# Kernel tuning notes

Hardware: AMD Instinct MI355X
Metric: run time of the kernel (lower is better)

The kernel has to match this reference:

```python
import jax, jax.numpy as jnp
import numpy as np

V, M, E, H = 20000, 32, 128, 4      # vocab, max news per word, embed dim, heads
N, L, C = 8192, 64, 128             # num news, max sent len, cnn out channels
KS = (3, 4, 5)


def setup_inputs() -> dict:
    key = jax.random.key(0)
    ks = jax.random.split(key, 12)
    s = 0.02
    return {
        "word2news": jax.random.randint(ks[0], (V, M), 0, N),
        "word2news_len": jax.random.randint(ks[1], (V,), 0, M),
        "news_words": jax.random.randint(ks[2], (N, L), 0, V),
        "news_embed_table": jax.random.normal(ks[3], (N, E), jnp.float32) * s,
        "in_proj_w": jax.random.normal(ks[4], (3 * E, E), jnp.float32) * s,
        "in_proj_b": jnp.zeros((3 * E,), jnp.float32),
        "out_proj_w": jax.random.normal(ks[5], (E, E), jnp.float32) * s,
        "out_proj_b": jnp.zeros((E,), jnp.float32),
        "conv_w3": jax.random.normal(ks[6], (C, E, 3), jnp.float32) * s,
        "conv_b3": jnp.zeros((C,), jnp.float32),
        "conv_w4": jax.random.normal(ks[7], (C, E, 4), jnp.float32) * s,
        "conv_b4": jnp.zeros((C,), jnp.float32),
        "conv_w5": jax.random.normal(ks[8], (C, E, 5), jnp.float32) * s,
        "conv_b5": jnp.zeros((C,), jnp.float32),
        "fc_w": jax.random.normal(ks[9], (E, len(KS) * C), jnp.float32) * s,
        "fc_b": jnp.zeros((E,), jnp.float32),
    }


def _conv1d(x, w, b):
    # x: [N, E, L]  w: [C, E, k]  -> [N, C, L-k+1]
    y = jax.lax.conv_general_dilated(x, w, (1,), "VALID",
                                     dimension_numbers=("NCH", "OIH", "NCH"))
    return y + b[None, :, None]


def _word_embeds(word2news, word2news_len, table, in_w, in_b, out_w, out_b):
    # Batched version of the per-word loop: masked mean query + 1-query MHA.
    mask = jnp.arange(M)[None, :] < word2news_len[:, None]          # [V, M]
    ctx = table[word2news]                                           # [V, M, E]
    cnt = jnp.maximum(word2news_len, 1).astype(ctx.dtype)[:, None]
    q = jnp.sum(jnp.where(mask[:, :, None], ctx, 0.0), axis=1) / cnt  # [V, E]
    wq, wk, wv = jnp.split(in_w, 3, axis=0)
    bq, bk, bv = jnp.split(in_b, 3, axis=0)
    Dh = E // H
    qh = (q @ wq.T + bq).reshape(V, H, Dh)
    kh = (ctx @ wk.T + bk).reshape(V, M, H, Dh)
    vh = (ctx @ wv.T + bv).reshape(V, M, H, Dh)
    scores = jnp.einsum("vhd,vmhd->vhm", qh, kh) / jnp.sqrt(jnp.asarray(Dh, ctx.dtype))
    scores = jnp.where(mask[:, None, :], scores, -1e9)
    attn = jax.nn.softmax(scores, axis=-1)
    o = jnp.einsum("vhm,vmhd->vhd", attn, vh).reshape(V, E)
    o = o @ out_w.T + out_b
    # words with no news stay zero, matching the zeros-init table in torch
    return jnp.where((word2news_len > 0)[:, None], o, 0.0)            # [V, E]


def reference(word2news, word2news_len, news_words, news_embed_table,
              in_proj_w, in_proj_b, out_proj_w, out_proj_b,
              conv_w3, conv_b3, conv_w4, conv_b4, conv_w5, conv_b5,
              fc_w, fc_b):
    word_embeds = _word_embeds(word2news, word2news_len, news_embed_table,
                               in_proj_w, in_proj_b, out_proj_w, out_proj_b)
    doc = word_embeds[news_words]                 # [N, L, E]
    x = doc.transpose(0, 2, 1)                    # [N, E, L]
    pooled = [jnp.max(jax.nn.relu(_conv1d(x, w, b)), axis=2)
              for w, b in ((conv_w3, conv_b3), (conv_w4, conv_b4), (conv_w5, conv_b5))]
    feats = jnp.concatenate(pooled, axis=1)       # [N, 3*C]; dropout=identity (eval)
    return feats @ fc_w.T + fc_b                  # [N, E]
```

## Files before the change

kernel.cpp:

```cpp
#include <hip/hip_runtime.h>
#include <math.h>

#define V_WORDS 20000
#define MM 32
#define EE 128
#define HH 4
#define DHH 32
#define NN 8192
#define LL 64
#define CC 128

typedef short bf16x8 __attribute__((ext_vector_type(8)));
typedef float f32x4 __attribute__((ext_vector_type(4)));
typedef unsigned short u16;
typedef unsigned int u32;

__device__ __forceinline__ u16 f2bf(float x) {
    u32 u = __float_as_uint(x);
    u32 r = (u + 0x7FFFu + ((u >> 16) & 1u)) >> 16;
    return (u16)r;
}
__device__ __forceinline__ float bflo(u32 u) { return __uint_as_float(u << 16); }
__device__ __forceinline__ float bfhi(u32 u) { return __uint_as_float(u & 0xFFFF0000u); }

__global__ __launch_bounds__(256)
void pack_weights(const float* __restrict__ w3,
                  const float* __restrict__ w4,
                  const float* __restrict__ w5,
                  u16* __restrict__ Bpack)
{
    const int s = blockIdx.x;
    const int t = threadIdx.x;
    const int lane = t & 63;

    const float* src;
    int K, sl;
    if (s < 12)      { src = w3; K = 3; sl = s; }
    else if (s < 28) { src = w4; K = 4; sl = s - 12; }
    else             { src = w5; K = 5; sl = s - 28; }
    const int j  = sl >> 2;
    const int e0 = (sl & 3) * 32;

    for (int nt = (t >> 6); nt < 8; nt += 4) {
        const int c = nt * 16 + (lane & 15);
        const int kb = (lane >> 4) * 8;
        u16 vals[8];
        #pragma unroll
        for (int i = 0; i < 8; ++i) {
            const int e = e0 + kb + i;
            vals[i] = f2bf(src[(c * EE + e) * K + j]);
        }
        u16* dst = Bpack + (((size_t)s * 8 + nt) * 64 + lane) * 8;
        *(bf16x8*)dst = *(const bf16x8*)vals;
    }
}

__global__ __launch_bounds__(256)
void kv_proj_kernel(const float* __restrict__ table,
                    const float* __restrict__ in_w,
                    const float* __restrict__ in_b,
                    u16* __restrict__ Kn16, u16* __restrict__ Vn16)
{
    const int n0 = blockIdx.x * 8;
    const int t = threadIdx.x;
    __shared__ float tbl[8][EE];
    {
        const int r = t >> 5, q4 = (t & 31) * 4;
        *(float4*)&tbl[r][q4] = *(const float4*)&table[(size_t)(n0 + r) * EE + q4];
    }
    __syncthreads();

    const int sel = t >> 7;
    const int i = t & 127;
    const float* w = in_w + (size_t)(sel + 1) * EE * EE + (size_t)i * EE;
    const float bias = in_b[(sel + 1) * EE + i];

    float acc[8];
    #pragma unroll
    for (int r = 0; r < 8; ++r) acc[r] = bias;
    for (int k = 0; k < EE; k += 4) {
        const float4 wv = *(const float4*)&w[k];
        #pragma unroll
        for (int r = 0; r < 8; ++r) {
            acc[r] += tbl[r][k]     * wv.x + tbl[r][k + 1] * wv.y
                    + tbl[r][k + 2] * wv.z + tbl[r][k + 3] * wv.w;
        }
    }
    u16* dst = sel ? Vn16 : Kn16;
    #pragma unroll
    for (int r = 0; r < 8; ++r) dst[(size_t)(n0 + r) * EE + i] = f2bf(acc[r]);
}

#define WPB 8
__global__ __launch_bounds__(256, 3)
void word_attn_kernel(const int* __restrict__ word2news,
                      const int* __restrict__ word2news_len,
                      const float* __restrict__ table,
                      const float* __restrict__ in_w,
                      const float* __restrict__ in_b,
                      const float* __restrict__ out_w,
                      const float* __restrict__ out_b,
                      const u16* __restrict__ Kn16,
                      const u16* __restrict__ Vn16,
                      u16* __restrict__ we16)
{
    const int v0 = blockIdx.x * WPB;
    const int t = threadIdx.x;

    __shared__ int   rows[WPB][MM];
    __shared__ int   lenS[WPB];
    __shared__ float q[WPB][EE];
    __shared__ float qh[WPB][EE];
    __shared__ float attn[WPB][HH][MM];
    __shared__ float osh[WPB][EE];

    {
        const int w = t >> 5, m = t & 31;
        rows[w][m] = word2news[(size_t)(v0 + w) * MM + m];
        if (t < WPB) lenS[t] = word2news_len[v0 + t];
    }
    __syncthreads();

    {
        const int w = t >> 5, d0 = (t & 31) * 4;
        const int L = lenS[w];
        float4 a = {0.f, 0.f, 0.f, 0.f};
        #pragma unroll 4
        for (int m = 0; m < MM; ++m) {
            const float4 x = *(const float4*)&table[(size_t)rows[w][m] * EE + d0];
            if (m < L) { a.x += x.x; a.y += x.y; a.z += x.z; a.w += x.w; }
        }
        const float inv = (L > 0) ? 1.0f / (float)L : 0.0f;
        a.x *= inv; a.y *= inv; a.z *= inv; a.w *= inv;
        *(float4*)&q[w][d0] = a;
    }
    __syncthreads();

    {
        const int g = t >> 7, i = t & 127;
        const float* wr = in_w + (size_t)i * EE;
        float acc[4] = {0.f, 0.f, 0.f, 0.f};
        #pragma unroll 4
        for (int k = 0; k < EE; k += 4) {
            const float4 wv = *(const float4*)&wr[k];
            #pragma unroll
            for (int w4 = 0; w4 < 4; ++w4) {
                const float* qw = q[g * 4 + w4];
                acc[w4] += qw[k] * wv.x + qw[k + 1] * wv.y
                         + qw[k + 2] * wv.z + qw[k + 3] * wv.w;
            }
        }
        const float b = in_b[i];
        #pragma unroll
        for (int w4 = 0; w4 < 4; ++w4) qh[g * 4 + w4][i] = acc[w4] + b;
    }
    __syncthreads();

    {
        const int w = t >> 5, m = t & 31;
        const int L = lenS[w];
        float s[HH] = {-1e9f, -1e9f, -1e9f, -1e9f};
        if (m < L) {
            const uint4* kr = (const uint4*)(Kn16 + (size_t)rows[w][m] * EE);
            #pragma unroll 1
            for (int h = 0; h < HH; ++h) {
                float a = 0.f;
                #pragma unroll
                for (int k8 = 0; k8 < 4; ++k8) {
                    const uint4 u = kr[h * 4 + k8];
                    const float4 q0 = *(const float4*)&qh[w][h * 32 + k8 * 8];
                    const float4 q1 = *(const float4*)&qh[w][h * 32 + k8 * 8 + 4];
                    a += q0.x * bflo(u.x) + q0.y * bfhi(u.x)
                       + q0.z * bflo(u.y) + q0.w * bfhi(u.y)
                       + q1.x * bflo(u.z) + q1.y * bfhi(u.z)
                       + q1.z * bflo(u.w) + q1.w * bfhi(u.w);
                }
                s[h] = a * 0.17677669529663687f;
            }
        }
        #pragma unroll
        for (int h = 0; h < HH; ++h) {
            float mx = s[h];
            #pragma unroll
            for (int off = 16; off > 0; off >>= 1)
                mx = fmaxf(mx, __shfl_xor(mx, off, 32));
            const float ex = expf(s[h] - mx);
            float sum = ex;
            #pragma unroll
            for (int off = 16; off > 0; off >>= 1)
                sum += __shfl_xor(sum, off, 32);
            attn[w][h][m] = ex / sum;
        }
    }
    __syncthreads();

    {
        const int w = t >> 5, d0 = (t & 31) * 4;
        const int h = d0 >> 5;
        float4 a = {0.f, 0.f, 0.f, 0.f};
        #pragma unroll 4
        for (int m = 0; m < MM; ++m) {
            const float aw = attn[w][h][m];
            const u32* vr = (const u32*)(Vn16 + (size_t)rows[w][m] * EE + d0);
            const u32 u0 = vr[0], u1 = vr[1];
            a.x += aw * bflo(u0); a.y += aw * bfhi(u0);
            a.z += aw * bflo(u1); a.w += aw * bfhi(u1);
        }
        *(float4*)&osh[w][d0] = a;
    }
    __syncthreads();

    {
        const int g = t >> 7, i = t & 127;
        const float* wr = out_w + (size_t)i * EE;
        float acc[4] = {0.f, 0.f, 0.f, 0.f};
        #pragma unroll 4
        for (int k = 0; k < EE; k += 4) {
            const float4 wv = *(const float4*)&wr[k];
            #pragma unroll
            for (int w4 = 0; w4 < 4; ++w4) {
                const float* ow = osh[g * 4 + w4];
                acc[w4] += ow[k] * wv.x + ow[k + 1] * wv.y
                         + ow[k + 2] * wv.z + ow[k + 3] * wv.w;
            }
        }
        const float b = out_b[i];
        #pragma unroll
        for (int w4 = 0; w4 < 4; ++w4) {
            const int w = g * 4 + w4;
            we16[(size_t)(v0 + w) * EE + i] =
                (lenS[w] > 0) ? f2bf(acc[w4] + b) : (u16)0;
        }
    }
}

#define DSTRIDE 136
#define DOCSZ   (68 * DSTRIDE)

template<int NSL, int SBASE, int NP>
__device__ __forceinline__ void conv_g2(const u16* __restrict__ lds,
                                        const u16* __restrict__ Bpack,
                                        const float* __restrict__ bk,
                                        int p, int nth, int l,
                                        float (&mxout)[4])
{
    f32x4 acc[4][4];
    #pragma unroll
    for (int mt = 0; mt < 4; ++mt)
        #pragma unroll
        for (int k = 0; k < 4; ++k)
            acc[mt][k] = (f32x4){0.f, 0.f, 0.f, 0.f};

    const int lm = l & 15;
    const int g  = l >> 4;
    const u16* bbase = Bpack + ((size_t)SBASE * 8 + nth * 4) * 512 + l * 8;
    const u16* abase = lds + (size_t)p * DOCSZ;

    #pragma unroll 2
    for (int s = 0; s < NSL; ++s) {
        const int j  = s >> 2;
        const int e0 = (s & 3) * 32;

        bf16x8 b[4];
        #pragma unroll
        for (int k = 0; k < 4; ++k)
            b[k] = *(const bf16x8*)(bbase + s * 4096 + k * 512);

        const u16* arow = abase + (lm + j) * DSTRIDE + e0 + g * 8;
        bf16x8 a[4];
        #pragma unroll
        for (int mt = 0; mt < 4; ++mt)
            a[mt] = *(const bf16x8*)(arow + mt * (16 * DSTRIDE));

        #pragma unroll
        for (int mt = 0; mt < 4; ++mt)
            #pragma unroll
            for (int k = 0; k < 4; ++k)
                acc[mt][k] = __builtin_amdgcn_mfma_f32_16x16x32_bf16(a[mt], b[k], acc[mt][k], 0, 0, 0);
    }

    #pragma unroll
    for (int k = 0; k < 4; ++k) {
        const int c = nth * 64 + k * 16 + lm;
        const float bias = bk[c];
        float mx = 0.0f;
        #pragma unroll
        for (int mt = 0; mt < 4; ++mt) {
            #pragma unroll
            for (int r = 0; r < 4; ++r) {
                const int pos = 16 * mt + g * 4 + r;
                const float y = fmaxf(acc[mt][k][r] + bias, 0.0f);
                if (pos < NP) mx = fmaxf(mx, y);
            }
        }
        mx = fmaxf(mx, __shfl_xor(mx, 16));
        mx = fmaxf(mx, __shfl_xor(mx, 32));
        mxout[k] = mx;
    }
}

__global__ __launch_bounds__(256, 4)
void news_kernel(const int* __restrict__ news_words,
                 const u16* __restrict__ we16,
                 const u16* __restrict__ Bpack,
                 const float* __restrict__ b3,
                 const float* __restrict__ b4,
                 const float* __restrict__ b5,
                 const float* __restrict__ fcw, const float* __restrict__ fcb,
                 float* __restrict__ out)
{
    const int n0 = blockIdx.x * 2;
    const int t = threadIdx.x;
    const int w = t >> 6, l = t & 63;
    const int p = w >> 1, nth = w & 1;

    __shared__ u16 lds[2 * DOCSZ];
    __shared__ int rows[2 * LL];

    if (t < 2 * LL) rows[t] = news_words[(size_t)n0 * LL + t];
    __syncthreads();

    {
        const uint4* weU = (const uint4*)we16;
        uint4* ldsU = (uint4*)lds;
        for (int idx = t; idx < 2048; idx += 256) {
            const int d = idx >> 10, rem = idx & 1023;
            const int row = rem >> 4, c4 = rem & 15;
            ldsU[d * 1156 + row * 17 + c4] = weU[(size_t)rows[d * 64 + row] * 16 + c4];
        }
        if (t < 128) {
            const int d = t >> 6, rem = t & 63;
            const int row = 64 + (rem >> 4), c4 = rem & 15;
            ldsU[d * 1156 + row * 17 + c4] = (uint4){0u, 0u, 0u, 0u};
        }
    }
    __syncthreads();

    float m3[4], m4[4], m5[4];
    conv_g2<12,  0, 62>(lds, Bpack, b3, p, nth, l, m3);
    conv_g2<16, 12, 61>(lds, Bpack, b4, p, nth, l, m4);
    conv_g2<20, 28, 60>(lds, Bpack, b5, p, nth, l, m5);
    __syncthreads();

    float* feats = (float*)lds;
    if ((l >> 4) == 0) {
        const int lm = l & 15;
        #pragma unroll
        for (int k = 0; k < 4; ++k) {
            const int c = nth * 64 + k * 16 + lm;
            feats[p * 384 +   0 + c] = m3[k];
            feats[p * 384 + 128 + c] = m4[k];
            feats[p * 384 + 256 + c] = m5[k];
        }
    }
    __syncthreads();

    if (t < 128) {
        const float4* wr4 = (const float4*)(fcw + (size_t)t * (3 * CC));
        float a0 = fcb[t], a1 = a0;
        for (int f4 = 0; f4 < 96; ++f4) {
            const float4 wv = wr4[f4];
            const float4 x0 = *(const float4*)&feats[0 * 384 + f4 * 4];
            const float4 x1 = *(const float4*)&feats[1 * 384 + f4 * 4];
            a0 += x0.x * wv.x + x0.y * wv.y + x0.z * wv.z + x0.w * wv.w;
            a1 += x1.x * wv.x + x1.y * wv.y + x1.z * wv.z + x1.w * wv.w;
        }
        out[(size_t)(n0 + 0) * EE + t] = a0;
        out[(size_t)(n0 + 1) * EE + t] = a1;
    }
}

extern "C" void kernel_launch(void* const* d_in, const int* in_sizes, int n_in,
                              void* d_out, int out_size, void* d_ws, size_t ws_size,
                              hipStream_t stream)
{
    const int*   word2news     = (const int*)d_in[0];
    const int*   word2news_len = (const int*)d_in[1];
    const int*   news_words    = (const int*)d_in[2];
    const float* table         = (const float*)d_in[3];
    const float* in_w          = (const float*)d_in[4];
    const float* in_b          = (const float*)d_in[5];
    const float* out_w         = (const float*)d_in[6];
    const float* out_b         = (const float*)d_in[7];
    const float* w3            = (const float*)d_in[8];
    const float* b3            = (const float*)d_in[9];
    const float* w4            = (const float*)d_in[10];
    const float* b4            = (const float*)d_in[11];
    const float* w5            = (const float*)d_in[12];
    const float* b5            = (const float*)d_in[13];
    const float* fcw           = (const float*)d_in[14];
    const float* fcb           = (const float*)d_in[15];

    float* out = (float*)d_out;
    u16* base  = (u16*)d_ws;
    u16* we16  = base;
    u16* Bpack = base + 2560000;
    u16* Kn16  = base + 2756608;
    u16* Vn16  = base + 3805184;

    pack_weights<<<48, 256, 0, stream>>>(w3, w4, w5, Bpack);
    kv_proj_kernel<<<NN / 8, 256, 0, stream>>>(table, in_w, in_b, Kn16, Vn16);
    word_attn_kernel<<<V_WORDS / WPB, 256, 0, stream>>>(
        word2news, word2news_len, table, in_w, in_b, out_w, out_b,
        Kn16, Vn16, we16);
    news_kernel<<<NN / 2, 256, 0, stream>>>(
        news_words, we16, Bpack, b3, b4, b5, fcw, fcb, out);
}
```

Baseline: 451.4 us.

## Precompute per-news Q projection and batch eight documents per news block

```diff
diff --git a/kernel.cpp b/kernel.cpp
--- a/kernel.cpp
+++ b/kernel.cpp
@@ -87,6 +87,44 @@
         }
     }
     u16* dst = sel ? Vn16 : Kn16;
+    #pragma unroll
+    for (int r = 0; r < 8; ++r) dst[(size_t)(n0 + r) * EE + i] = f2bf(acc[r]);
+}
+
+__global__ __launch_bounds__(384)
+void kvq_proj_kernel(const float* __restrict__ table,
+                     const float* __restrict__ in_w,
+                     const float* __restrict__ in_b,
+                     u16* __restrict__ Qn16,
+                     u16* __restrict__ Kn16,
+                     u16* __restrict__ Vn16)
+{
+    const int n0 = blockIdx.x * 8;
+    const int t = threadIdx.x;
+    __shared__ float tbl[8][EE];
+    if (t < 256) {
+        const int r = t >> 5, q4 = (t & 31) * 4;
+        *(float4*)&tbl[r][q4] = *(const float4*)&table[(size_t)(n0 + r) * EE + q4];
+    }
+    __syncthreads();
+
+    const int sel = t >> 7;
+    const int i = t & 127;
+    const float* w = in_w + (size_t)sel * EE * EE + (size_t)i * EE;
+    const float bias = in_b[sel * EE + i];
+
+    float acc[8];
+    #pragma unroll
+    for (int r = 0; r < 8; ++r) acc[r] = bias;
+    for (int k = 0; k < EE; k += 4) {
+        const float4 wv = *(const float4*)&w[k];
+        #pragma unroll
+        for (int r = 0; r < 8; ++r) {
+            acc[r] += tbl[r][k]     * wv.x + tbl[r][k + 1] * wv.y
+                    + tbl[r][k + 2] * wv.z + tbl[r][k + 3] * wv.w;
+        }
+    }
+    u16* dst = (sel == 0) ? Qn16 : (sel == 1) ? Kn16 : Vn16;
     #pragma unroll
     for (int r = 0; r < 8; ++r) dst[(size_t)(n0 + r) * EE + i] = f2bf(acc[r]);
 }
@@ -234,6 +272,129 @@
     }
 }
 
+__global__ __launch_bounds__(256, 3)
+void word_attn_qn(const int* __restrict__ word2news,
+                  const int* __restrict__ word2news_len,
+                  const float* __restrict__ out_w,
+                  const float* __restrict__ out_b,
+                  const u16* __restrict__ Qn16,
+                  const u16* __restrict__ Kn16,
+                  const u16* __restrict__ Vn16,
+                  u16* __restrict__ we16)
+{
+    const int v0 = blockIdx.x * WPB;
+    const int t = threadIdx.x;
+
+    __shared__ int   rows[WPB][MM];
+    __shared__ int   lenS[WPB];
+    __shared__ float qh[WPB][EE];
+    __shared__ float attn[WPB][HH][MM];
+    __shared__ float osh[WPB][EE];
+
+    {
+        const int w = t >> 5, m = t & 31;
+        rows[w][m] = word2news[(size_t)(v0 + w) * MM + m];
+        if (t < WPB) lenS[t] = word2news_len[v0 + t];
+    }
+    __syncthreads();
+
+    {
+        const int w = t >> 5, d0 = (t & 31) * 4;
+        const int L = lenS[w];
+        float4 a = {0.f, 0.f, 0.f, 0.f};
+        #pragma unroll 4
+        for (int m = 0; m < MM; ++m) {
+            const u32* qr = (const u32*)(Qn16 + (size_t)rows[w][m] * EE + d0);
+            const u32 u0 = qr[0], u1 = qr[1];
+            if (m < L) {
+                a.x += bflo(u0); a.y += bfhi(u0);
+                a.z += bflo(u1); a.w += bfhi(u1);
+            }
+        }
+        const float inv = (L > 0) ? 1.0f / (float)L : 0.0f;
+        a.x *= inv; a.y *= inv; a.z *= inv; a.w *= inv;
+        *(float4*)&qh[w][d0] = a;
+    }
+    __syncthreads();
+
+    {
+        const int w = t >> 5, m = t & 31;
+        const int L = lenS[w];
+        float s[HH] = {-1e9f, -1e9f, -1e9f, -1e9f};
+        if (m < L) {
+            const uint4* kr = (const uint4*)(Kn16 + (size_t)rows[w][m] * EE);
+            #pragma unroll 1
+            for (int h = 0; h < HH; ++h) {
+                float a = 0.f;
+                #pragma unroll
+                for (int k8 = 0; k8 < 4; ++k8) {
+                    const uint4 u = kr[h * 4 + k8];
+                    const float4 q0 = *(const float4*)&qh[w][h * 32 + k8 * 8];
+                    const float4 q1 = *(const float4*)&qh[w][h * 32 + k8 * 8 + 4];
+                    a += q0.x * bflo(u.x) + q0.y * bfhi(u.x)
+                       + q0.z * bflo(u.y) + q0.w * bfhi(u.y)
+                       + q1.x * bflo(u.z) + q1.y * bfhi(u.z)
+                       + q1.z * bflo(u.w) + q1.w * bfhi(u.w);
+                }
+                s[h] = a * 0.17677669529663687f;
+            }
+        }
+        #pragma unroll
+        for (int h = 0; h < HH; ++h) {
+            float mx = s[h];
+            #pragma unroll
+            for (int off = 16; off > 0; off >>= 1)
+                mx = fmaxf(mx, __shfl_xor(mx, off, 32));
+            const float ex = expf(s[h] - mx);
+            float sum = ex;
+            #pragma unroll
+            for (int off = 16; off > 0; off >>= 1)
+                sum += __shfl_xor(sum, off, 32);
+            attn[w][h][m] = ex / sum;
+        }
+    }
+    __syncthreads();
+
+    {
+        const int w = t >> 5, d0 = (t & 31) * 4;
+        const int h = d0 >> 5;
+        float4 a = {0.f, 0.f, 0.f, 0.f};
+        #pragma unroll 4
+        for (int m = 0; m < MM; ++m) {
+            const float aw = attn[w][h][m];
+            const u32* vr = (const u32*)(Vn16 + (size_t)rows[w][m] * EE + d0);
+            const u32 u0 = vr[0], u1 = vr[1];
+            a.x += aw * bflo(u0); a.y += aw * bfhi(u0);
+            a.z += aw * bflo(u1); a.w += aw * bfhi(u1);
+        }
+        *(float4*)&osh[w][d0] = a;
+    }
+    __syncthreads();
+
+    {
+        const int g = t >> 7, i = t & 127;
+        const float* wr = out_w + (size_t)i * EE;
+        float acc[4] = {0.f, 0.f, 0.f, 0.f};
+        #pragma unroll 4
+        for (int k = 0; k < EE; k += 4) {
+            const float4 wv = *(const float4*)&wr[k];
+            #pragma unroll
+            for (int w4 = 0; w4 < 4; ++w4) {
+                const float* ow = osh[g * 4 + w4];
+                acc[w4] += ow[k] * wv.x + ow[k + 1] * wv.y
+                         + ow[k + 2] * wv.z + ow[k + 3] * wv.w;
+            }
+        }
+        const float b = out_b[i];
+        #pragma unroll
+        for (int w4 = 0; w4 < 4; ++w4) {
+            const int w = g * 4 + w4;
+            we16[(size_t)(v0 + w) * EE + i] =
+                (lenS[w] > 0) ? f2bf(acc[w4] + b) : (u16)0;
+        }
+    }
+}
+
 #define DSTRIDE 136
 #define DOCSZ   (68 * DSTRIDE)
 
@@ -299,7 +460,7 @@
     }
 }
 
-__global__ __launch_bounds__(256, 4)
+__global__ __launch_bounds__(1024, 4)
 void news_kernel(const int* __restrict__ news_words,
                  const u16* __restrict__ we16,
                  const u16* __restrict__ Bpack,
@@ -309,26 +470,26 @@
                  const float* __restrict__ fcw, const float* __restrict__ fcb,
                  float* __restrict__ out)
 {
-    const int n0 = blockIdx.x * 2;
+    const int n0 = blockIdx.x * 8;
     const int t = threadIdx.x;
     const int w = t >> 6, l = t & 63;
     const int p = w >> 1, nth = w & 1;
 
-    __shared__ u16 lds[2 * DOCSZ];
-    __shared__ int rows[2 * LL];
-
-    if (t < 2 * LL) rows[t] = news_words[(size_t)n0 * LL + t];
+    __shared__ u16 lds[8 * DOCSZ];
+    __shared__ int rows[8 * LL];
+
+    if (t < 8 * LL) rows[t] = news_words[(size_t)n0 * LL + t];
     __syncthreads();
 
     {
         const uint4* weU = (const uint4*)we16;
         uint4* ldsU = (uint4*)lds;
-        for (int idx = t; idx < 2048; idx += 256) {
+        for (int idx = t; idx < 8192; idx += 1024) {
             const int d = idx >> 10, rem = idx & 1023;
             const int row = rem >> 4, c4 = rem & 15;
             ldsU[d * 1156 + row * 17 + c4] = weU[(size_t)rows[d * 64 + row] * 16 + c4];
         }
-        if (t < 128) {
+        if (t < 512) {
             const int d = t >> 6, rem = t & 63;
             const int row = 64 + (rem >> 4), c4 = rem & 15;
             ldsU[d * 1156 + row * 17 + c4] = (uint4){0u, 0u, 0u, 0u};
@@ -357,16 +518,20 @@
 
     if (t < 128) {
         const float4* wr4 = (const float4*)(fcw + (size_t)t * (3 * CC));
-        float a0 = fcb[t], a1 = a0;
+        float a[8];
+        #pragma unroll
+        for (int d = 0; d < 8; ++d) a[d] = fcb[t];
         for (int f4 = 0; f4 < 96; ++f4) {
             const float4 wv = wr4[f4];
-            const float4 x0 = *(const float4*)&feats[0 * 384 + f4 * 4];
-            const float4 x1 = *(const float4*)&feats[1 * 384 + f4 * 4];
-            a0 += x0.x * wv.x + x0.y * wv.y + x0.z * wv.z + x0.w * wv.w;
-            a1 += x1.x * wv.x + x1.y * wv.y + x1.z * wv.z + x1.w * wv.w;
-        }
-        out[(size_t)(n0 + 0) * EE + t] = a0;
-        out[(size_t)(n0 + 1) * EE + t] = a1;
+            #pragma unroll
+            for (int d = 0; d < 8; ++d) {
+                const float4 x = *(const float4*)&feats[d * 384 + f4 * 4];
+                a[d] += x.x * wv.x + x.y * wv.y + x.z * wv.z + x.w * wv.w;
+            }
+        }
+        #pragma unroll
+        for (int d = 0; d < 8; ++d)
+            out[(size_t)(n0 + d) * EE + t] = a[d];
     }
 }
 
@@ -397,12 +562,23 @@
     u16* Bpack = base + 2560000;
     u16* Kn16  = base + 2756608;
     u16* Vn16  = base + 3805184;
+    u16* Qn16  = base + 4853760;
+    const size_t need_qn = (size_t)(4853760 + 1048576) * 2;
 
     pack_weights<<<48, 256, 0, stream>>>(w3, w4, w5, Bpack);
-    kv_proj_kernel<<<NN / 8, 256, 0, stream>>>(table, in_w, in_b, Kn16, Vn16);
-    word_attn_kernel<<<V_WORDS / WPB, 256, 0, stream>>>(
-        word2news, word2news_len, table, in_w, in_b, out_w, out_b,
-        Kn16, Vn16, we16);
-    news_kernel<<<NN / 2, 256, 0, stream>>>(
+
+    if (ws_size >= need_qn) {
+        kvq_proj_kernel<<<NN / 8, 384, 0, stream>>>(table, in_w, in_b,
+                                                    Qn16, Kn16, Vn16);
+        word_attn_qn<<<V_WORDS / WPB, 256, 0, stream>>>(
+            word2news, word2news_len, out_w, out_b, Qn16, Kn16, Vn16, we16);
+    } else {
+        kv_proj_kernel<<<NN / 8, 256, 0, stream>>>(table, in_w, in_b, Kn16, Vn16);
+        word_attn_kernel<<<V_WORDS / WPB, 256, 0, stream>>>(
+            word2news, word2news_len, table, in_w, in_b, out_w, out_b,
+            Kn16, Vn16, we16);
+    }
+
+    news_kernel<<<NN / 8, 1024, 0, stream>>>(
         news_words, we16, Bpack, b3, b4, b5, fcw, fcb, out);
 }
```

New measurement: 518.2 us. +14.8%, slower.
